# Optimization experiments

Measured on AMD Instinct MI355X. Metric: run time of the kernel, lower is better.

Reference implementation:

```python
import jax, jax.numpy as jnp
import numpy as np

T, B, IN_DIM, HID = 512, 64, 512, 1024


def setup_inputs() -> dict:
    key = jax.random.key(0)
    ks = jax.random.split(key, 9)
    s_in = 1.0 / np.sqrt(IN_DIM + HID)  # torch Linear default init scale
    inputs = jax.random.normal(ks[0], (T, B, IN_DIM), dtype=jnp.float32)
    def w(k):
        return jax.random.uniform(k, (IN_DIM + HID, HID), jnp.float32, -s_in, s_in)
    def b(k):
        return jax.random.uniform(k, (HID,), jnp.float32, -s_in, s_in)
    return {
        "inputs": inputs,
        "Wf": w(ks[1]), "bf": b(ks[2]),
        "Wi": w(ks[3]), "bi": b(ks[4]),
        "Wg": w(ks[5]), "bg": b(ks[6]),
        "Wo": w(ks[7]), "bo": b(ks[8]),
    }


def _lstm(inputs, Wf, bf, Wi, bi, Wg, bg, Wo, bo):
    # Fuse the 4 gate linears into one GEMM: [in+hid, 4*hid]
    W = jnp.concatenate([Wf, Wi, Wg, Wo], axis=1)
    bias = jnp.concatenate([bf, bi, bg, bo], axis=0)
    batch = inputs.shape[1]
    h0 = jnp.zeros((batch, HID), inputs.dtype)
    c0 = jnp.zeros((batch, HID), inputs.dtype)

    def step(carry, x):
        hx, cx = carry
        combined = jnp.concatenate([x, hx], axis=1)  # [B, in+hid]
        z = combined @ W + bias                       # [B, 4*hid]
        f = jax.nn.sigmoid(z[:, 0 * HID:1 * HID])
        i = jax.nn.sigmoid(z[:, 1 * HID:2 * HID])
        g = jnp.tanh(z[:, 2 * HID:3 * HID])
        o = jax.nn.sigmoid(z[:, 3 * HID:4 * HID])
        cx = f * cx + i * g
        hx = o * jnp.tanh(cx)
        return (hx, cx), hx

    (hx, cx), stacked = jax.lax.scan(step, (h0, c0), inputs)
    return stacked, hx, cx


def reference(inputs, Wf, bf, Wi, bi, Wg, bg, Wo, bo):
    return _lstm(inputs, Wf, bf, Wi, bi, Wg, bg, Wo, bo)
```

## Files before the change

kernel.cpp:

```cpp
#include <hip/hip_runtime.h>
#include <math.h>


namespace {

constexpr int T_STEPS = 512;
constexpr int B = 64;
constexpr int IN = 512;
constexpr int H = 1024;
constexpr int K = IN + H;
constexpr int NBLK = 256;
constexpr int NXMF = IN / 32;
constexpr int NHMF = H / 32;
constexpr int WPITCH = K + 8;
constexpr int HPITCH = H + 8;

constexpr size_t HBUF_OFF = 0;
constexpr size_t XBUF_OFF = HBUF_OFF + 2ull * B * H * 2;
constexpr size_t BAR_OFF = XBUF_OFF + 2ull * B * IN * 2;
constexpr size_t COMBX_OFF = BAR_OFF + 1056ull * 4;
constexpr size_t NEED_PRE = COMBX_OFF + (size_t)T_STEPS * B * IN * 2;

typedef __attribute__((ext_vector_type(8))) _Float16 f16x8;
typedef __attribute__((ext_vector_type(4))) float f32x4;

__device__ __forceinline__ f16x8 load_sc1_16B(const _Float16* p) {
  union {
    unsigned long long u[2];
    f16x8 v;
  } cv;
  const unsigned long long* q = (const unsigned long long*)p;
  cv.u[0] = __hip_atomic_load(q, __ATOMIC_RELAXED, __HIP_MEMORY_SCOPE_AGENT);
  cv.u[1] =
      __hip_atomic_load(q + 1, __ATOMIC_RELAXED, __HIP_MEMORY_SCOPE_AGENT);
  return cv.v;
}

__device__ __forceinline__ void store_sc1_u64(_Float16* p,
                                              unsigned long long v) {
  __hip_atomic_store((unsigned long long*)p, v, __ATOMIC_RELAXED,
                     __HIP_MEMORY_SCOPE_AGENT);
}

__device__ __forceinline__ void store_sc1_u32(unsigned* p, unsigned v) {
  __hip_atomic_store(p, v, __ATOMIC_RELAXED, __HIP_MEMORY_SCOPE_AGENT);
}

__device__ __forceinline__ float fast_sigmoid(float z) {
  return __builtin_amdgcn_rcpf(1.0f + __expf(-z));
}
__device__ __forceinline__ float fast_tanh(float z) {
  return 1.0f - 2.0f * __builtin_amdgcn_rcpf(1.0f + __expf(2.0f * z));
}

__global__ void prep_pre(const float* __restrict__ x,
                         _Float16* __restrict__ combx,
                         _Float16* __restrict__ hbuf,
                         unsigned* __restrict__ bar) {
  const size_t i = (size_t)blockIdx.x * 256 + threadIdx.x;
  if (i < (size_t)T_STEPS * B * IN) combx[i] = (_Float16)x[i];
  if (i < 2ull * B * H) hbuf[i] = (_Float16)0.f;
  if (i < 1056) bar[i] = 0u;
}

__global__ void prep_fb(const float* __restrict__ x,
                        _Float16* __restrict__ xbuf,
                        _Float16* __restrict__ hbuf,
                        unsigned* __restrict__ bar) {
  const size_t i = (size_t)blockIdx.x * 256 + threadIdx.x;
  if (i < (size_t)B * IN) xbuf[i] = (_Float16)x[i];
  if (i < 2ull * B * H) hbuf[i] = (_Float16)0.f;
  if (i < 1056) bar[i] = 0u;
}

template <bool PRE>
__global__ __launch_bounds__(256, 1) void lstm_persist(
    const float* __restrict__ x, const float* __restrict__ Wf,
    const float* __restrict__ Wi, const float* __restrict__ Wg,
    const float* __restrict__ Wo, const float* __restrict__ bf,
    const float* __restrict__ bi_, const float* __restrict__ bg,
    const float* __restrict__ bo, float* __restrict__ out,
    _Float16* __restrict__ combx, _Float16* __restrict__ xbuf,
    _Float16* __restrict__ hbuf, unsigned* __restrict__ bar) {
  __shared__ _Float16 Wlds[16 * WPITCH];
  __shared__ _Float16 Hlds[16 * HPITCH];

  const int blk = blockIdx.x;
  const int tid = threadIdx.x;
  const int bgrp = blk & 3;
  const int jgrp = blk >> 2;
  const int jbase = jgrp * 16;

  const int lane = tid & 63;
  const int wv = tid >> 6;
  const int q = lane >> 4;
  const int n = lane & 15;
  const int gate = n >> 2;
  const int jj = n & 3;
  const int j0w = jbase + wv * 4;
  const int brow0 = bgrp * 16;

  f16x8 Bfrag[NXMF + NHMF];
  {
    const float* wptr[4] = {Wf, Wi, Wg, Wo};
    for (int c = 0; c < 4; ++c) {
#pragma unroll
      for (int g = 0; g < 4; ++g) {
        const float* wsrc = wptr[g];
        for (int it = 0; it < K / 256; ++it) {
          const int k = it * 256 + tid;
          const float4 w =
              *(const float4*)(wsrc + (size_t)k * H + jbase + c * 4);
          Wlds[(g * 4 + 0) * WPITCH + k] = (_Float16)w.x;
          Wlds[(g * 4 + 1) * WPITCH + k] = (_Float16)w.y;
          Wlds[(g * 4 + 2) * WPITCH + k] = (_Float16)w.z;
          Wlds[(g * 4 + 3) * WPITCH + k] = (_Float16)w.w;
        }
      }
      __syncthreads();
      if (wv == c) {
#pragma unroll
        for (int kk = 0; kk < NXMF + NHMF; ++kk) {
          Bfrag[kk] = *(const f16x8*)(&Wlds[n * WPITCH + kk * 32 + q * 8]);
        }
      }
      __syncthreads();
    }
  }

  const float* bptr[4] = {bf, bi_, bg, bo};
  const float bias_v = bptr[gate][j0w + jj];

  float c_reg[4] = {0.f, 0.f, 0.f, 0.f};

  unsigned* flags = bar + bgrp * 64;

  f32x4 acc_x;
  auto xpart = [&](int t) {
    f32x4 a = {bias_v, bias_v, bias_v, bias_v};
    f32x4 b = {0.f, 0.f, 0.f, 0.f};
    if constexpr (PRE) {
      const _Float16* ab =
          combx + (size_t)t * B * IN + (size_t)(brow0 + n) * IN + q * 8;
#pragma unroll
      for (int kk = 0; kk < NXMF; kk += 2) {
        f16x8 f0 = *(const f16x8*)(ab + kk * 32);
        f16x8 f1 = *(const f16x8*)(ab + (kk + 1) * 32);
        a = __builtin_amdgcn_mfma_f32_16x16x32_f16(f0, Bfrag[kk], a, 0, 0, 0);
        b = __builtin_amdgcn_mfma_f32_16x16x32_f16(f1, Bfrag[kk + 1], b, 0, 0,
                                                   0);
      }
    } else {
      const _Float16* ab =
          xbuf + (size_t)(t & 1) * B * IN + (size_t)(brow0 + n) * IN + q * 8;
#pragma unroll
      for (int kk = 0; kk < NXMF; kk += 2) {
        f16x8 f0 = load_sc1_16B(ab + kk * 32);
        f16x8 f1 = load_sc1_16B(ab + (kk + 1) * 32);
        a = __builtin_amdgcn_mfma_f32_16x16x32_f16(f0, Bfrag[kk], a, 0, 0, 0);
        b = __builtin_amdgcn_mfma_f32_16x16x32_f16(f1, Bfrag[kk + 1], b, 0, 0,
                                                   0);
      }
    }
    acc_x = a + b;
  };

  xpart(0);

  for (int t = 0; t < T_STEPS; ++t) {
    const _Float16* hb = hbuf + (size_t)(t & 1) * B * H + (size_t)brow0 * H;
    _Float16* hb_next = hbuf + (size_t)((t + 1) & 1) * B * H;

    f16x8 va[4], vb[4];
#pragma unroll
    for (int i = 0; i < 4; ++i) {
      const int g = tid + i * 256;
      const int row = g >> 6;
      const int c16 = g & 63;
      va[i] = load_sc1_16B(hb + (size_t)row * H + c16 * 8);
    }
#pragma unroll
    for (int i = 0; i < 4; ++i) {
      const int g = tid + i * 256;
      const int row = g >> 6;
      const int c16 = g & 63;
      vb[i] = load_sc1_16B(hb + (size_t)row * H + 512 + c16 * 8);
    }
#pragma unroll
    for (int i = 0; i < 4; ++i) {
      const int g = tid + i * 256;
      const int row = g >> 6;
      const int c16 = g & 63;
      *(f16x8*)(&Hlds[row * HPITCH + c16 * 8]) = va[i];
    }
    __syncthreads();

    f32x4 a0 = acc_x;
    f32x4 a1 = {0.f, 0.f, 0.f, 0.f};
    f32x4 a2 = {0.f, 0.f, 0.f, 0.f};
    f32x4 a3 = {0.f, 0.f, 0.f, 0.f};
    {
      const _Float16* hl = &Hlds[n * HPITCH + q * 8];
#pragma unroll
      for (int kk = 0; kk < NHMF / 2; kk += 4) {
        f16x8 f0 = *(const f16x8*)(hl + kk * 32);
        f16x8 f1 = *(const f16x8*)(hl + (kk + 1) * 32);
        f16x8 f2 = *(const f16x8*)(hl + (kk + 2) * 32);
        f16x8 f3 = *(const f16x8*)(hl + (kk + 3) * 32);
        a0 = __builtin_amdgcn_mfma_f32_16x16x32_f16(f0, Bfrag[NXMF + kk], a0,
                                                    0, 0, 0);
        a1 = __builtin_amdgcn_mfma_f32_16x16x32_f16(f1, Bfrag[NXMF + kk + 1],
                                                    a1, 0, 0, 0);
        a2 = __builtin_amdgcn_mfma_f32_16x16x32_f16(f2, Bfrag[NXMF + kk + 2],
                                                    a2, 0, 0, 0);
        a3 = __builtin_amdgcn_mfma_f32_16x16x32_f16(f3, Bfrag[NXMF + kk + 3],
                                                    a3, 0, 0, 0);
      }
    }
#pragma unroll
    for (int i = 0; i < 4; ++i) {
      const int g = tid + i * 256;
      const int row = g >> 6;
      const int c16 = g & 63;
      *(f16x8*)(&Hlds[row * HPITCH + 512 + c16 * 8]) = vb[i];
    }
    __syncthreads();
    {
      const _Float16* hl = &Hlds[n * HPITCH + q * 8];
#pragma unroll
      for (int kk = NHMF / 2; kk < NHMF; kk += 4) {
        f16x8 f0 = *(const f16x8*)(hl + kk * 32);
        f16x8 f1 = *(const f16x8*)(hl + (kk + 1) * 32);
        f16x8 f2 = *(const f16x8*)(hl + (kk + 2) * 32);
        f16x8 f3 = *(const f16x8*)(hl + (kk + 3) * 32);
        a0 = __builtin_amdgcn_mfma_f32_16x16x32_f16(f0, Bfrag[NXMF + kk], a0,
                                                    0, 0, 0);
        a1 = __builtin_amdgcn_mfma_f32_16x16x32_f16(f1, Bfrag[NXMF + kk + 1],
                                                    a1, 0, 0, 0);
        a2 = __builtin_amdgcn_mfma_f32_16x16x32_f16(f2, Bfrag[NXMF + kk + 2],
                                                    a2, 0, 0, 0);
        a3 = __builtin_amdgcn_mfma_f32_16x16x32_f16(f3, Bfrag[NXMF + kk + 3],
                                                    a3, 0, 0, 0);
      }
    }
    const f32x4 acc = (a0 + a1) + (a2 + a3);

    float v[4];
#pragma unroll
    for (int r = 0; r < 4; ++r) {
      const float z = acc[r];
      v[r] = (gate == 2) ? fast_tanh(z) : fast_sigmoid(z);
    }
    float vi[4], vg[4], vo[4];
#pragma unroll
    for (int r = 0; r < 4; ++r) {
      vi[r] = __shfl(v[r], (lane + 4) & 63, 64);
      vg[r] = __shfl(v[r], (lane + 8) & 63, 64);
      vo[r] = __shfl(v[r], (lane + 12) & 63, 64);
    }
    float hv[4];
#pragma unroll
    for (int r = 0; r < 4; ++r) {
      const float c = fmaf(v[r], c_reg[r], vi[r] * vg[r]);
      c_reg[r] = c;
      hv[r] = vo[r] * fast_tanh(c);
    }
    float h1[4], h2[4], h3[4];
#pragma unroll
    for (int r = 0; r < 4; ++r) {
      h1[r] = __shfl(hv[r], (lane + 1) & 63, 64);
      h2[r] = __shfl(hv[r], (lane + 2) & 63, 64);
      h3[r] = __shfl(hv[r], (lane + 3) & 63, 64);
    }
    if (n == 0) {
#pragma unroll
      for (int r = 0; r < 4; ++r) {
        const int b = brow0 + q * 4 + r;
        union {
          _Float16 h[4];
          unsigned long long u;
        } pk;
        pk.h[0] = (_Float16)hv[r];
        pk.h[1] = (_Float16)h1[r];
        pk.h[2] = (_Float16)h2[r];
        pk.h[3] = (_Float16)h3[r];
        store_sc1_u64(hb_next + (size_t)b * H + j0w, pk.u);
      }
    }

    if (!PRE && t + 1 < T_STEPS && tid < 16) {
      _Float16* xn = xbuf + (size_t)((t + 1) & 1) * B * IN;
      const int row = brow0 + (jgrp >> 2);
      const int off = (jgrp & 3) * 128 + tid * 8;
      const float* xs = x + (size_t)(t + 1) * B * IN + (size_t)row * IN + off;
      const float4 x0 = *(const float4*)xs;
      const float4 x1 = *(const float4*)(xs + 4);
      float vals[8] = {x0.x, x0.y, x0.z, x0.w, x1.x, x1.y, x1.z, x1.w};
#pragma unroll
      for (int i = 0; i < 4; ++i) {
        union {
          _Float16 h[2];
          unsigned u;
        } pk;
        pk.h[0] = (_Float16)vals[2 * i];
        pk.h[1] = (_Float16)vals[2 * i + 1];
        store_sc1_u32((unsigned*)(xn + (size_t)row * IN + off + 2 * i), pk.u);
      }
    }

    if (t + 1 < T_STEPS) {
      __syncthreads();
      if (tid == 0) store_sc1_u32(flags + jgrp, (unsigned)(t + 1));
      if (n == 0) {
#pragma unroll
        for (int r = 0; r < 4; ++r) {
          const int b = brow0 + q * 4 + r;
          const float4 o4 = make_float4(hv[r], h1[r], h2[r], h3[r]);
          *(float4*)(out + (size_t)t * B * H + (size_t)b * H + j0w) = o4;
        }
      }
      if (PRE) xpart(t + 1);
      if (wv == 0) {
        const unsigned tgt = (unsigned)(t + 1);
        for (;;) {
          const unsigned f = __hip_atomic_load(flags + lane, __ATOMIC_RELAXED,
                                               __HIP_MEMORY_SCOPE_AGENT);
          if (__all(f >= tgt)) break;
          __builtin_amdgcn_s_sleep(1);
        }
      }
      asm volatile("" ::: "memory");
      __builtin_amdgcn_s_barrier();
      asm volatile("" ::: "memory");
      if (!PRE) xpart(t + 1);
    } else {
      float c1[4], c2[4], c3[4];
#pragma unroll
      for (int r = 0; r < 4; ++r) {
        c1[r] = __shfl(c_reg[r], (lane + 1) & 63, 64);
        c2[r] = __shfl(c_reg[r], (lane + 2) & 63, 64);
        c3[r] = __shfl(c_reg[r], (lane + 3) & 63, 64);
      }
      if (n == 0) {
#pragma unroll
        for (int r = 0; r < 4; ++r) {
          const int b = brow0 + q * 4 + r;
          const float4 o4 = make_float4(hv[r], h1[r], h2[r], h3[r]);
          *(float4*)(out + (size_t)t * B * H + (size_t)b * H + j0w) = o4;
          *(float4*)(out + (size_t)T_STEPS * B * H + (size_t)b * H + j0w) =
              o4;
          const float4 c4 = make_float4(c_reg[r], c1[r], c2[r], c3[r]);
          *(float4*)(out + (size_t)T_STEPS * B * H + (size_t)B * H +
                     (size_t)b * H + j0w) = c4;
        }
      }
    }
  }
}

}

extern "C" void kernel_launch(void* const* d_in, const int* in_sizes, int n_in,
                              void* d_out, int out_size, void* d_ws,
                              size_t ws_size, hipStream_t stream) {
  const float* x = (const float*)d_in[0];
  const float* Wf = (const float*)d_in[1];
  const float* bf = (const float*)d_in[2];
  const float* Wi = (const float*)d_in[3];
  const float* bi = (const float*)d_in[4];
  const float* Wg = (const float*)d_in[5];
  const float* bg = (const float*)d_in[6];
  const float* Wo = (const float*)d_in[7];
  const float* bo = (const float*)d_in[8];
  float* out = (float*)d_out;

  char* ws = (char*)d_ws;
  _Float16* hbuf = (_Float16*)(ws + HBUF_OFF);
  _Float16* xbuf = (_Float16*)(ws + XBUF_OFF);
  unsigned* bar = (unsigned*)(ws + BAR_OFF);
  _Float16* combx = (_Float16*)(ws + COMBX_OFF);

  const bool pre = ws_size >= NEED_PRE;

  if (pre) {
    const size_t n = (size_t)T_STEPS * B * IN;
    prep_pre<<<(unsigned)((n + 255) / 256), 256, 0, stream>>>(x, combx, hbuf,
                                                              bar);
    lstm_persist<true><<<NBLK, 256, 0, stream>>>(
        x, Wf, Wi, Wg, Wo, bf, bi, bg, bo, out, combx, xbuf, hbuf, bar);
  } else {
    prep_fb<<<(2 * B * H + 255) / 256, 256, 0, stream>>>(x, xbuf, hbuf, bar);
    lstm_persist<false><<<NBLK, 256, 0, stream>>>(
        x, Wf, Wi, Wg, Wo, bf, bi, bg, bo, out, combx, xbuf, hbuf, bar);
  }
}
```

Baseline: 3.392 ms.

## Tag h-state words with step number so consumers poll data directly

Each fp16 hidden value is stored as a 32-bit word that pairs the value with a 16-bit step tag. Consumer blocks can then check the tag and accept data as soon as it arrives, rather than relying only on the flag barrier. The first half of h is prefetched before the barrier wait, and the second half is loaded and validated while the first-half MFMAs run. This is meant to shorten the per-step critical path of the cross-block barrier, at the cost of doubling h-buffer traffic and adding spin-retry loops on the data.

```diff
diff --git a/kernel.cpp b/kernel.cpp
--- a/kernel.cpp
+++ b/kernel.cpp
@@ -16,7 +16,7 @@
 constexpr int HPITCH = H + 8;
 
 constexpr size_t HBUF_OFF = 0;
-constexpr size_t XBUF_OFF = HBUF_OFF + 2ull * B * H * 2;
+constexpr size_t XBUF_OFF = HBUF_OFF + 2ull * B * H * 4;
 constexpr size_t BAR_OFF = XBUF_OFF + 2ull * B * IN * 2;
 constexpr size_t COMBX_OFF = BAR_OFF + 1056ull * 4;
 constexpr size_t NEED_PRE = COMBX_OFF + (size_t)T_STEPS * B * IN * 2;
@@ -36,10 +36,9 @@
   return cv.v;
 }
 
-__device__ __forceinline__ void store_sc1_u64(_Float16* p,
-                                              unsigned long long v) {
-  __hip_atomic_store((unsigned long long*)p, v, __ATOMIC_RELAXED,
-                     __HIP_MEMORY_SCOPE_AGENT);
+__device__ __forceinline__ void store_sc1_u64p(unsigned long long* p,
+                                               unsigned long long v) {
+  __hip_atomic_store(p, v, __ATOMIC_RELAXED, __HIP_MEMORY_SCOPE_AGENT);
 }
 
 __device__ __forceinline__ void store_sc1_u32(unsigned* p, unsigned v) {
@@ -55,21 +54,21 @@
 
 __global__ void prep_pre(const float* __restrict__ x,
                          _Float16* __restrict__ combx,
-                         _Float16* __restrict__ hbuf,
+                         unsigned* __restrict__ hbuf,
                          unsigned* __restrict__ bar) {
   const size_t i = (size_t)blockIdx.x * 256 + threadIdx.x;
   if (i < (size_t)T_STEPS * B * IN) combx[i] = (_Float16)x[i];
-  if (i < 2ull * B * H) hbuf[i] = (_Float16)0.f;
+  if (i < 2ull * B * H) hbuf[i] = 0u;
   if (i < 1056) bar[i] = 0u;
 }
 
 __global__ void prep_fb(const float* __restrict__ x,
                         _Float16* __restrict__ xbuf,
-                        _Float16* __restrict__ hbuf,
+                        unsigned* __restrict__ hbuf,
                         unsigned* __restrict__ bar) {
   const size_t i = (size_t)blockIdx.x * 256 + threadIdx.x;
   if (i < (size_t)B * IN) xbuf[i] = (_Float16)x[i];
-  if (i < 2ull * B * H) hbuf[i] = (_Float16)0.f;
+  if (i < 2ull * B * H) hbuf[i] = 0u;
   if (i < 1056) bar[i] = 0u;
 }
 
@@ -81,7 +80,7 @@
     const float* __restrict__ bi_, const float* __restrict__ bg,
     const float* __restrict__ bo, float* __restrict__ out,
     _Float16* __restrict__ combx, _Float16* __restrict__ xbuf,
-    _Float16* __restrict__ hbuf, unsigned* __restrict__ bar) {
+    unsigned* __restrict__ hbuf, unsigned* __restrict__ bar) {
   __shared__ _Float16 Wlds[16 * WPITCH];
   __shared__ _Float16 Hlds[16 * HPITCH];
 
@@ -135,6 +134,49 @@
 
   unsigned* flags = bar + bgrp * 64;
 
+  auto issue_half = [&](const unsigned* hb32, int halfBase, uint4* v,
+                        unsigned pend) {
+#pragma unroll
+    for (int i = 0; i < 8; ++i)
+      if (pend & (1u << i)) {
+        const int g2 = tid + i * 256;
+        const int row = g2 >> 7;
+        const int cg = g2 & 127;
+        const unsigned* p = hb32 + (size_t)row * H + halfBase + cg * 4;
+        const unsigned long long u0 = __hip_atomic_load(
+            (const unsigned long long*)p, __ATOMIC_RELAXED,
+            __HIP_MEMORY_SCOPE_AGENT);
+        const unsigned long long u1 = __hip_atomic_load(
+            (const unsigned long long*)p + 1, __ATOMIC_RELAXED,
+            __HIP_MEMORY_SCOPE_AGENT);
+        v[i].x = (unsigned)u0;
+        v[i].y = (unsigned)(u0 >> 32);
+        v[i].z = (unsigned)u1;
+        v[i].w = (unsigned)(u1 >> 32);
+      }
+  };
+  auto check_half = [&](int halfBase, uint4* v, unsigned tag,
+                        unsigned& pend) {
+#pragma unroll
+    for (int i = 0; i < 8; ++i)
+      if (pend & (1u << i)) {
+        const uint4 t4 = v[i];
+        const bool ok =
+            ((t4.x & 0xFFFFu) == tag) & ((t4.y & 0xFFFFu) == tag) &
+            ((t4.z & 0xFFFFu) == tag) & ((t4.w & 0xFFFFu) == tag);
+        if (ok) {
+          const int g2 = tid + i * 256;
+          const int row = g2 >> 7;
+          const int cg = g2 & 127;
+          const unsigned lo = (t4.x >> 16) | (t4.y & 0xFFFF0000u);
+          const unsigned hi = (t4.z >> 16) | (t4.w & 0xFFFF0000u);
+          *(unsigned long long*)(&Hlds[row * HPITCH + halfBase + cg * 4]) =
+              (unsigned long long)lo | ((unsigned long long)hi << 32);
+          pend &= ~(1u << i);
+        }
+      }
+  };
+
   f32x4 acc_x;
   auto xpart = [&](int t) {
     f32x4 a = {bias_v, bias_v, bias_v, bias_v};
@@ -167,33 +209,29 @@
 
   xpart(0);
 
+  uint4 vA[8];
+  unsigned pendA = 0xFFu;
+  {
+    const unsigned* hb32 = hbuf + (size_t)brow0 * H;
+    issue_half(hb32, 0, vA, pendA);
+    check_half(0, vA, 0u, pendA);
+  }
+
   for (int t = 0; t < T_STEPS; ++t) {
-    const _Float16* hb = hbuf + (size_t)(t & 1) * B * H + (size_t)brow0 * H;
-    _Float16* hb_next = hbuf + (size_t)((t + 1) & 1) * B * H;
-
-    f16x8 va[4], vb[4];
-#pragma unroll
-    for (int i = 0; i < 4; ++i) {
-      const int g = tid + i * 256;
-      const int row = g >> 6;
-      const int c16 = g & 63;
-      va[i] = load_sc1_16B(hb + (size_t)row * H + c16 * 8);
-    }
-#pragma unroll
-    for (int i = 0; i < 4; ++i) {
-      const int g = tid + i * 256;
-      const int row = g >> 6;
-      const int c16 = g & 63;
-      vb[i] = load_sc1_16B(hb + (size_t)row * H + 512 + c16 * 8);
-    }
-#pragma unroll
-    for (int i = 0; i < 4; ++i) {
-      const int g = tid + i * 256;
-      const int row = g >> 6;
-      const int c16 = g & 63;
-      *(f16x8*)(&Hlds[row * HPITCH + c16 * 8]) = va[i];
+    const unsigned tagt = (unsigned)t;
+    const unsigned* hb32 =
+        hbuf + (size_t)(t & 1) * B * H + (size_t)brow0 * H;
+
+    while (pendA) {
+      issue_half(hb32, 0, vA, pendA);
+      check_half(0, vA, tagt, pendA);
+      if (pendA) __builtin_amdgcn_s_sleep(1);
     }
     __syncthreads();
+
+    uint4 vB[8];
+    unsigned pendB = 0xFFu;
+    issue_half(hb32, 512, vB, pendB);
 
     f32x4 a0 = acc_x;
     f32x4 a1 = {0.f, 0.f, 0.f, 0.f};
@@ -217,14 +255,15 @@
                                                     a3, 0, 0, 0);
       }
     }
-#pragma unroll
-    for (int i = 0; i < 4; ++i) {
-      const int g = tid + i * 256;
-      const int row = g >> 6;
-      const int c16 = g & 63;
-      *(f16x8*)(&Hlds[row * HPITCH + 512 + c16 * 8]) = vb[i];
+
+    check_half(512, vB, tagt, pendB);
+    while (pendB) {
+      issue_half(hb32, 512, vB, pendB);
+      check_half(512, vB, tagt, pendB);
+      if (pendB) __builtin_amdgcn_s_sleep(1);
     }
     __syncthreads();
+
     {
       const _Float16* hl = &Hlds[n * HPITCH + q * 8];
 #pragma unroll
@@ -273,18 +312,29 @@
       h3[r] = __shfl(hv[r], (lane + 3) & 63, 64);
     }
     if (n == 0) {
+      const unsigned tag = (unsigned)(t + 1) & 0xFFFFu;
+      unsigned* hn = hbuf + (size_t)((t + 1) & 1) * B * H;
 #pragma unroll
       for (int r = 0; r < 4; ++r) {
         const int b = brow0 + q * 4 + r;
         union {
-          _Float16 h[4];
-          unsigned long long u;
-        } pk;
-        pk.h[0] = (_Float16)hv[r];
-        pk.h[1] = (_Float16)h1[r];
-        pk.h[2] = (_Float16)h2[r];
-        pk.h[3] = (_Float16)h3[r];
-        store_sc1_u64(hb_next + (size_t)b * H + j0w, pk.u);
+          _Float16 f;
+          unsigned short s;
+        } c0, c1, c2, c3;
+        c0.f = (_Float16)hv[r];
+        c1.f = (_Float16)h1[r];
+        c2.f = (_Float16)h2[r];
+        c3.f = (_Float16)h3[r];
+        const unsigned w0 = ((unsigned)c0.s << 16) | tag;
+        const unsigned w1 = ((unsigned)c1.s << 16) | tag;
+        const unsigned w2 = ((unsigned)c2.s << 16) | tag;
+        const unsigned w3 = ((unsigned)c3.s << 16) | tag;
+        unsigned long long* p =
+            (unsigned long long*)(hn + (size_t)b * H + j0w);
+        store_sc1_u64p(p, (unsigned long long)w0 |
+                              ((unsigned long long)w1 << 32));
+        store_sc1_u64p(p + 1, (unsigned long long)w2 |
+                                  ((unsigned long long)w3 << 32));
       }
     }
 
@@ -309,7 +359,13 @@
     }
 
     if (t + 1 < T_STEPS) {
-      __syncthreads();
+      if (PRE) {
+        asm volatile("" ::: "memory");
+        __builtin_amdgcn_s_barrier();
+        asm volatile("" ::: "memory");
+      } else {
+        __syncthreads();
+      }
       if (tid == 0) store_sc1_u32(flags + jgrp, (unsigned)(t + 1));
       if (n == 0) {
 #pragma unroll
@@ -320,6 +376,13 @@
         }
       }
       if (PRE) xpart(t + 1);
+      {
+        const unsigned* hn32 =
+            hbuf + (size_t)((t + 1) & 1) * B * H + (size_t)brow0 * H;
+        pendA = 0xFFu;
+        issue_half(hn32, 0, vA, pendA);
+        check_half(0, vA, (unsigned)(t + 1) & 0xFFFFu, pendA);
+      }
       if (wv == 0) {
         const unsigned tgt = (unsigned)(t + 1);
         for (;;) {
@@ -375,7 +438,7 @@
   float* out = (float*)d_out;
 
   char* ws = (char*)d_ws;
-  _Float16* hbuf = (_Float16*)(ws + HBUF_OFF);
+  unsigned* hbuf = (unsigned*)(ws + HBUF_OFF);
   _Float16* xbuf = (_Float16*)(ws + XBUF_OFF);
   unsigned* bar = (unsigned*)(ws + BAR_OFF);
   _Float16* combx = (_Float16*)(ws + COMBX_OFF);
```

Measured after the change: 3.802 ms. 1.12x slower.
